# Optimization experiments

Hardware: AMD Instinct MI355X
Metric: run time of the kernel (lower is better)

Reference implementation:

```python
import jax, jax.numpy as jnp
import numpy as np

B, S, E = 1, 2048, 2048
HQ, HKV = 32, 8
D = E // HQ            # 64 head dim
REP = HQ // HKV        # 4 q-heads per kv-head
NEG = -1e9


def _rope(t, fr, fi):
    # t: [B,S,H,D]; fr/fi: [S,D//2] real/imag of unit complex freqs
    tr = t.reshape(*t.shape[:-1], D // 2, 2)
    t0, t1 = tr[..., 0], tr[..., 1]
    fr = fr[None, :, None, :]
    fi = fi[None, :, None, :]
    out = jnp.stack([t0 * fr - t1 * fi, t0 * fi + t1 * fr], axis=-1)
    return out.reshape(t.shape)


def setup_inputs() -> dict:
    key = jax.random.key(0)
    kx, kq, kk, kv, ko = jax.random.split(key, 5)
    x = jax.random.normal(kx, (B, S, E), dtype=jnp.float32)
    # standard RoPE frequencies: theta = 10000^{-2i/D}
    inv_freq = 1.0 / (10000.0 ** (np.arange(0, D, 2, dtype=np.float32) / D))
    ang = np.arange(S, dtype=np.float32)[:, None] * inv_freq[None, :]  # [S, D//2]
    freqs_cis = jnp.asarray(np.stack([np.cos(ang), np.sin(ang)], axis=-1))  # [S,D//2,2]
    # causal additive mask [S,S]
    mask = jnp.where(np.tril(np.ones((S, S), dtype=bool)), 0.0, NEG).astype(jnp.float32)
    s = 1.0 / np.sqrt(E)
    Wq = jax.random.normal(kq, (E, HQ * D), dtype=jnp.float32) * s
    Wk = jax.random.normal(kk, (E, HKV * D), dtype=jnp.float32) * s
    Wv = jax.random.normal(kv, (E, HKV * D), dtype=jnp.float32) * s
    Wo = jax.random.normal(ko, (HQ * D, E), dtype=jnp.float32) * s
    return {"x": x, "freqs_cis": freqs_cis, "mask": mask,
            "Wq": Wq, "Wk": Wk, "Wv": Wv, "Wo": Wo}


def reference(x, freqs_cis, mask, Wq, Wk, Wv, Wo):
    b, s, _ = x.shape
    xq = (x @ Wq).reshape(b, s, HQ, D)
    xk = (x @ Wk).reshape(b, s, HKV, D)
    xv = (x @ Wv).reshape(b, s, HKV, D)
    fr, fi = freqs_cis[..., 0], freqs_cis[..., 1]
    xq = _rope(xq, fr, fi)
    xk = _rope(xk, fr, fi)
    # explicit GQA kv-head repeat (matches torch repeat+view)
    xk = jnp.repeat(xk, REP, axis=2)  # [b,s,HQ,D]
    xv = jnp.repeat(xv, REP, axis=2)
    q = xq.transpose(0, 2, 1, 3)  # [b,h,s,d]
    k = xk.transpose(0, 2, 1, 3)
    v = xv.transpose(0, 2, 1, 3)
    scores = jnp.einsum('bhqd,bhkd->bhqk', q, k) / jnp.sqrt(jnp.float32(D))
    scores = scores + mask[None, None]
    probs = jax.nn.softmax(scores, axis=-1)
    attn = jnp.einsum('bhqk,bhkd->bhqd', probs, v)
    attn = attn.transpose(0, 2, 1, 3).reshape(b, s, HQ * D)
    return attn @ Wo
```

## Files before the change

kernel.cpp:

```cpp
#include <hip/hip_runtime.h>
#include <stdint.h>

#define SEQ   2048
#define EDIM  2048
#define NHQ   32
#define NHKV  8
#define HDIM  64
#define NQKV  3072

#define LOG2E 1.4426950408889634f

typedef __bf16 bf16x8 __attribute__((ext_vector_type(8)));
typedef float  f32x4  __attribute__((ext_vector_type(4)));

typedef __attribute__((address_space(1))) void gvoid;
typedef __attribute__((address_space(3))) void lvoid;

__device__ __forceinline__ unsigned short f2bf(float f) {
  unsigned int u = __builtin_bit_cast(unsigned int, f);
  u += 0x7FFFu + ((u >> 16) & 1u);
  return (unsigned short)(u >> 16);
}

__device__ __forceinline__ unsigned int pk2bf(float lo, float hi) {
  return (unsigned)f2bf(lo) | ((unsigned)f2bf(hi) << 16);
}

__device__ __forceinline__ float fexp2(float x) {
#if __has_builtin(__builtin_amdgcn_exp2f)
  return __builtin_amdgcn_exp2f(x);
#else
  return exp2f(x);
#endif
}

__device__ __forceinline__ bf16x8 ld_g16(const unsigned short* p) {
  uint4 u = *reinterpret_cast<const uint4*>(p);
  return __builtin_bit_cast(bf16x8, u);
}

__device__ __forceinline__ void stage16(const void* g, void* l) {
  __builtin_amdgcn_global_load_lds((gvoid*)g, (lvoid*)l, 16, 0, 0);
}

__global__ __launch_bounds__(256) void conv_x_kernel(
    const float* __restrict__ x, unsigned short* __restrict__ xb) {
  int i = (blockIdx.x * 256 + threadIdx.x) * 8;
  float4 a = *reinterpret_cast<const float4*>(x + i);
  float4 b = *reinterpret_cast<const float4*>(x + i + 4);
  uint4 o;
  o.x = pk2bf(a.x, a.y);
  o.y = pk2bf(a.z, a.w);
  o.z = pk2bf(b.x, b.y);
  o.w = pk2bf(b.z, b.w);
  *reinterpret_cast<uint4*>(xb + i) = o;
}

__global__ __launch_bounds__(256) void tr_qkv_kernel(
    const float* __restrict__ Wq, const float* __restrict__ Wk,
    const float* __restrict__ Wv, unsigned short* __restrict__ Bt) {
  __shared__ float tile[32][33];
  const int tx = threadIdx.x, ty = threadIdx.y;
  const int kb = blockIdx.x * 32, nb = blockIdx.y * 32;
#pragma unroll
  for (int i = 0; i < 4; ++i) {
    int k = kb + ty + i * 8;
    int n = nb + tx;
    float v;
    if (n < 2048)      v = Wq[k * 2048 + n];
    else if (n < 2560) v = Wk[k * 512 + (n - 2048)];
    else               v = Wv[k * 512 + (n - 2560)];
    tile[ty + i * 8][tx] = v;
  }
  __syncthreads();
#pragma unroll
  for (int i = 0; i < 4; ++i) {
    int n = nb + ty + i * 8;
    int k = kb + tx;
    Bt[n * 2048 + k] = f2bf(tile[tx][ty + i * 8]);
  }
}

__global__ __launch_bounds__(256) void tr_wo_kernel(
    const float* __restrict__ Wo, unsigned short* __restrict__ Bt) {
  __shared__ float tile[32][33];
  const int tx = threadIdx.x, ty = threadIdx.y;
  const int kb = blockIdx.x * 32, nb = blockIdx.y * 32;
#pragma unroll
  for (int i = 0; i < 4; ++i)
    tile[ty + i * 8][tx] = Wo[(kb + ty + i * 8) * 2048 + nb + tx];
  __syncthreads();
#pragma unroll
  for (int i = 0; i < 4; ++i)
    Bt[(nb + ty + i * 8) * 2048 + kb + tx] = f2bf(tile[tx][ty + i * 8]);
}

template <int MODE>
__global__ __launch_bounds__(256) void gemm_kernel(
    const unsigned short* __restrict__ A, const unsigned short* __restrict__ Bt,
    const float* __restrict__ freqs, unsigned short* __restrict__ Qb,
    unsigned short* __restrict__ Kb, unsigned short* __restrict__ VT,
    float* __restrict__ Cout, int N_, int K) {
  __shared__ alignas(16) unsigned short As[2][128 * 32];
  __shared__ alignas(16) unsigned short Bs[2][128 * 32];
  const int t = threadIdx.x;
  const int w = t >> 6, l = t & 63;
  const int q = l >> 4, r16 = l & 15;
  const int wr = w >> 1, wc = w & 1;
  const int brow = blockIdx.x * 128, bcol = blockIdx.y * 128;
  const unsigned short* Arow = A + (size_t)brow * K;
  const unsigned short* Brow = Bt + (size_t)bcol * K;
  const int sg0 = t, sg1 = 256 + t;
  f32x4 acc[4][4] = {};

  {
    stage16(Arow + (sg0 >> 2) * K + (sg0 & 3) * 8, (char*)As[0] + sg0 * 16);
    stage16(Brow + (sg0 >> 2) * K + (sg0 & 3) * 8, (char*)Bs[0] + sg0 * 16);
    stage16(Arow + (sg1 >> 2) * K + (sg1 & 3) * 8, (char*)As[0] + sg1 * 16);
    stage16(Brow + (sg1 >> 2) * K + (sg1 & 3) * 8, (char*)Bs[0] + sg1 * 16);
  }
  __syncthreads();

  for (int kt = 0; kt < K; kt += 32) {
    const int cur = (kt >> 5) & 1;
    if (kt + 32 < K) {
      const int nkt = kt + 32;
      stage16(Arow + (sg0 >> 2) * K + nkt + (sg0 & 3) * 8,
              (char*)As[cur ^ 1] + sg0 * 16);
      stage16(Brow + (sg0 >> 2) * K + nkt + (sg0 & 3) * 8,
              (char*)Bs[cur ^ 1] + sg0 * 16);
      stage16(Arow + (sg1 >> 2) * K + nkt + (sg1 & 3) * 8,
              (char*)As[cur ^ 1] + sg1 * 16);
      stage16(Brow + (sg1 >> 2) * K + nkt + (sg1 & 3) * 8,
              (char*)Bs[cur ^ 1] + sg1 * 16);
    }
    bf16x8 af[4], bfr[4];
#pragma unroll
    for (int mf = 0; mf < 4; ++mf)
      af[mf] = *(const bf16x8*)(As[cur] + (wr * 64 + mf * 16 + r16) * 32 + q * 8);
#pragma unroll
    for (int nf = 0; nf < 4; ++nf)
      bfr[nf] = *(const bf16x8*)(Bs[cur] + (wc * 64 + nf * 16 + r16) * 32 + q * 8);
#pragma unroll
    for (int mf = 0; mf < 4; ++mf)
#pragma unroll
      for (int nf = 0; nf < 4; ++nf)
        acc[mf][nf] = __builtin_amdgcn_mfma_f32_16x16x32_bf16(
            af[mf], bfr[nf], acc[mf][nf], 0, 0, 0);
    __syncthreads();
  }

#pragma unroll
  for (int mf = 0; mf < 4; ++mf) {
#pragma unroll
    for (int nf = 0; nf < 4; ++nf) {
      int j = bcol + wc * 64 + nf * 16 + r16;
#pragma unroll
      for (int reg = 0; reg < 4; ++reg) {
        float v = acc[mf][nf][reg];
        int srow = brow + wr * 64 + mf * 16 + q * 4 + reg;
        if (MODE == 1) {
          Cout[(size_t)srow * N_ + j] = v;
        } else {
          float pv = __shfl_xor(v, 1);
          int d = j & 63;
          if (j < 2048) {
            float2 f = *reinterpret_cast<const float2*>(
                freqs + ((size_t)srow * 32 + (d >> 1)) * 2);
            float ov = (d & 1) ? (pv * f.y + v * f.x) : (v * f.x - pv * f.y);
            Qb[(size_t)(j >> 6) * (SEQ * HDIM) + srow * HDIM + d] =
                f2bf(ov * (0.125f * LOG2E));
          } else if (j < 2560) {
            float2 f = *reinterpret_cast<const float2*>(
                freqs + ((size_t)srow * 32 + (d >> 1)) * 2);
            float ov = (d & 1) ? (pv * f.y + v * f.x) : (v * f.x - pv * f.y);
            Kb[(size_t)((j - 2048) >> 6) * (SEQ * HDIM) + srow * HDIM + d] =
                f2bf(ov);
          } else {
            VT[(size_t)((j - 2560) >> 6) * (HDIM * SEQ) + d * SEQ + srow] =
                f2bf(v);
          }
        }
      }
    }
  }
}

__global__ __launch_bounds__(64, 3) void flash_kernel(
    const unsigned short* __restrict__ Qb, const unsigned short* __restrict__ Kb,
    const unsigned short* __restrict__ VT, unsigned short* __restrict__ attnb) {
  const int bi = blockIdx.x;
  const int h = bi & 31, hk = h >> 2;
  const int qc = 63 - (bi >> 5);
  const int l = threadIdx.x & 63;
  const int hi = l >> 4, r16 = l & 15;
  const int qrow0 = qc * 32;
  const unsigned short* Qh = Qb + (size_t)h * (SEQ * HDIM);
  const unsigned short* Kh = Kb + (size_t)hk * (SEQ * HDIM);
  const unsigned short* Vh = VT + (size_t)hk * (HDIM * SEQ);

  bf16x8 qf[2][2];
#pragma unroll
  for (int mf = 0; mf < 2; ++mf)
#pragma unroll
    for (int ks = 0; ks < 2; ++ks)
      qf[mf][ks] = ld_g16(Qh + (qrow0 + mf * 16 + r16) * HDIM + ks * 32 + hi * 8);

  f32x4 o[2][4] = {};
  float mrow[2] = {-1e9f, -1e9f};
  float lrow[2] = {0.f, 0.f};

  const int nkv = (qc >> 2) + 1;
  for (int kv = 0; kv < nkv; ++kv) {
    const int kvbase = kv * 128;
    f32x4 s[2][8] = {};
#pragma unroll
    for (int nf = 0; nf < 8; ++nf) {
      const unsigned short* kp =
          Kh + (size_t)(kvbase + nf * 16 + r16) * HDIM + hi * 8;
      bf16x8 a0 = ld_g16(kp);
      bf16x8 a1 = ld_g16(kp + 32);
      s[0][nf] = __builtin_amdgcn_mfma_f32_16x16x32_bf16(a0, qf[0][0], s[0][nf], 0, 0, 0);
      s[1][nf] = __builtin_amdgcn_mfma_f32_16x16x32_bf16(a0, qf[1][0], s[1][nf], 0, 0, 0);
      s[0][nf] = __builtin_amdgcn_mfma_f32_16x16x32_bf16(a1, qf[0][1], s[0][nf], 0, 0, 0);
      s[1][nf] = __builtin_amdgcn_mfma_f32_16x16x32_bf16(a1, qf[1][1], s[1][nf], 0, 0, 0);
    }
    if (kv == nkv - 1) {
#pragma unroll
      for (int mf = 0; mf < 2; ++mf) {
        int qr = qrow0 + mf * 16 + r16;
#pragma unroll
        for (int nf = 0; nf < 8; ++nf) {
          int kc = kvbase + nf * 16 + hi * 4;
#pragma unroll
          for (int r = 0; r < 4; ++r)
            if (kc + r > qr) s[mf][nf][r] = -1e9f;
        }
      }
    }
    float mx[2];
#pragma unroll
    for (int mf = 0; mf < 2; ++mf) {
      f32x4 m4 = s[mf][0];
#pragma unroll
      for (int nf = 1; nf < 8; ++nf) {
        m4[0] = fmaxf(m4[0], s[mf][nf][0]); m4[1] = fmaxf(m4[1], s[mf][nf][1]);
        m4[2] = fmaxf(m4[2], s[mf][nf][2]); m4[3] = fmaxf(m4[3], s[mf][nf][3]);
      }
      float v = fmaxf(fmaxf(m4[0], m4[1]), fmaxf(m4[2], m4[3]));
      v = fmaxf(v, __shfl_xor(v, 16));
      v = fmaxf(v, __shfl_xor(v, 32));
      mx[mf] = v;
    }
    if (!__all(fmaxf(mx[0] - mrow[0], mx[1] - mrow[1]) <= 8.0f)) {
#pragma unroll
      for (int mf = 0; mf < 2; ++mf) {
        float mn = fmaxf(mrow[mf], mx[mf]);
        float al = fexp2(mrow[mf] - mn);
        mrow[mf] = mn;
        lrow[mf] *= al;
#pragma unroll
        for (int r = 0; r < 4; ++r) {
          float alr = __shfl(al, hi * 4 + r);
#pragma unroll
          for (int nd = 0; nd < 4; ++nd) o[mf][nd][r] *= alr;
        }
      }
    }
#pragma unroll
    for (int mf = 0; mf < 2; ++mf) {
      f32x4 a4 = {0.f, 0.f, 0.f, 0.f};
#pragma unroll
      for (int nf = 0; nf < 8; ++nf) {
#pragma unroll
        for (int r = 0; r < 4; ++r) {
          float p = fexp2(s[mf][nf][r] - mrow[mf]);
          s[mf][nf][r] = p;
          a4[r] += p;
        }
      }
      float rs = (a4[0] + a4[1]) + (a4[2] + a4[3]);
      rs += __shfl_xor(rs, 16);
      rs += __shfl_xor(rs, 32);
      lrow[mf] += rs;
    }
#pragma unroll
    for (int kt = 0; kt < 8; ++kt) {
      bf16x8 pa[2];
#pragma unroll
      for (int mf = 0; mf < 2; ++mf) {
        bf16x8 p = {};
        p[0] = (__bf16)s[mf][kt][0];
        p[1] = (__bf16)s[mf][kt][1];
        p[2] = (__bf16)s[mf][kt][2];
        p[3] = (__bf16)s[mf][kt][3];
        pa[mf] = p;
      }
#pragma unroll
      for (int nd = 0; nd < 4; ++nd) {
        uint2 v2 = *reinterpret_cast<const uint2*>(
            Vh + (size_t)(nd * 16 + r16) * SEQ + kvbase + kt * 16 + hi * 4);
        uint4 u; u.x = v2.x; u.y = v2.y; u.z = 0u; u.w = 0u;
        bf16x8 vb = __builtin_bit_cast(bf16x8, u);
        o[0][nd] = __builtin_amdgcn_mfma_f32_16x16x32_bf16(pa[0], vb, o[0][nd], 0, 0, 0);
        o[1][nd] = __builtin_amdgcn_mfma_f32_16x16x32_bf16(pa[1], vb, o[1][nd], 0, 0, 0);
      }
    }
  }
#pragma unroll
  for (int mf = 0; mf < 2; ++mf) {
    float linv = 1.0f / lrow[mf];
#pragma unroll
    for (int r = 0; r < 4; ++r) {
      float lr = __shfl(linv, hi * 4 + r);
      int srow = qrow0 + mf * 16 + hi * 4 + r;
#pragma unroll
      for (int nd = 0; nd < 4; ++nd) {
        int d = nd * 16 + r16;
        attnb[(size_t)srow * 2048 + h * 64 + d] = f2bf(o[mf][nd][r] * lr);
      }
    }
  }
}

extern "C" void kernel_launch(void* const* d_in, const int* in_sizes, int n_in,
                              void* d_out, int out_size, void* d_ws,
                              size_t ws_size, hipStream_t stream) {
  const float* x     = (const float*)d_in[0];
  const float* freqs = (const float*)d_in[1];
  const float* Wq = (const float*)d_in[3];
  const float* Wk = (const float*)d_in[4];
  const float* Wv = (const float*)d_in[5];
  const float* Wo = (const float*)d_in[6];
  float* out = (float*)d_out;
  char* ws = (char*)d_ws;
  const size_t MB = 1024 * 1024;
  unsigned short* xb    = (unsigned short*)(ws);
  unsigned short* WqkvT = (unsigned short*)(ws + 8 * MB);
  unsigned short* WoT   = (unsigned short*)(ws + 20 * MB);
  unsigned short* Qbuf  = (unsigned short*)(ws + 28 * MB);
  unsigned short* Kbuf  = (unsigned short*)(ws + 36 * MB);
  unsigned short* Vt    = (unsigned short*)(ws + 38 * MB);
  unsigned short* attnb = (unsigned short*)(ws + 40 * MB);

  conv_x_kernel<<<dim3(2048), dim3(256), 0, stream>>>(x, xb);
  tr_qkv_kernel<<<dim3(64, 96), dim3(32, 8), 0, stream>>>(Wq, Wk, Wv, WqkvT);
  tr_wo_kernel<<<dim3(64, 64), dim3(32, 8), 0, stream>>>(Wo, WoT);
  gemm_kernel<0><<<dim3(16, 24), dim3(256), 0, stream>>>(
      xb, WqkvT, freqs, Qbuf, Kbuf, Vt, (float*)nullptr, NQKV, 2048);
  flash_kernel<<<dim3(2048), dim3(64), 0, stream>>>(Qbuf, Kbuf, Vt, attnb);
  gemm_kernel<1><<<dim3(16, 16), dim3(256), 0, stream>>>(
      attnb, WoT, (const float*)nullptr, (unsigned short*)nullptr,
      (unsigned short*)nullptr, (unsigned short*)nullptr, out, 2048, 2048);
}
```

Baseline: 357.2 us.

## Retile GEMMs to 128x64 with K=64 steps, XOR-swizzled LDS, XCD block remap

The projection GEMMs now use 128x64 output tiles with a 64-deep K step instead of 128x128 with a 32-deep step. The LDS layout gets an XOR swizzle to avoid bank conflicts. A 1D grid is remapped so consecutive tiles land on the same XCD, which should improve L2 reuse. Smaller N tiles double the block count (768/512), which fills the 256 CUs better, at the cost of less register reuse per block.

```diff
diff --git a/kernel.cpp b/kernel.cpp
--- a/kernel.cpp
+++ b/kernel.cpp
@@ -100,61 +100,73 @@
     const unsigned short* __restrict__ A, const unsigned short* __restrict__ Bt,
     const float* __restrict__ freqs, unsigned short* __restrict__ Qb,
     unsigned short* __restrict__ Kb, unsigned short* __restrict__ VT,
-    float* __restrict__ Cout, int N_, int K) {
-  __shared__ alignas(16) unsigned short As[2][128 * 32];
-  __shared__ alignas(16) unsigned short Bs[2][128 * 32];
+    float* __restrict__ Cout, int N_, int K, int nwg) {
+  __shared__ alignas(16) unsigned short As[2][128 * 64];
+  __shared__ alignas(16) unsigned short Bs[2][64 * 64];
   const int t = threadIdx.x;
   const int w = t >> 6, l = t & 63;
   const int q = l >> 4, r16 = l & 15;
   const int wr = w >> 1, wc = w & 1;
-  const int brow = blockIdx.x * 128, bcol = blockIdx.y * 128;
+  const int cpx = nwg >> 3;
+  const int id = (blockIdx.x & 7) * cpx + (blockIdx.x >> 3);
+  const int brow = (id & 15) * 128;
+  const int bcol = (id >> 4) * 64;
   const unsigned short* Arow = A + (size_t)brow * K;
   const unsigned short* Brow = Bt + (size_t)bcol * K;
-  const int sg0 = t, sg1 = 256 + t;
-  f32x4 acc[4][4] = {};
-
-  {
-    stage16(Arow + (sg0 >> 2) * K + (sg0 & 3) * 8, (char*)As[0] + sg0 * 16);
-    stage16(Brow + (sg0 >> 2) * K + (sg0 & 3) * 8, (char*)Bs[0] + sg0 * 16);
-    stage16(Arow + (sg1 >> 2) * K + (sg1 & 3) * 8, (char*)As[0] + sg1 * 16);
-    stage16(Brow + (sg1 >> 2) * K + (sg1 & 3) * 8, (char*)Bs[0] + sg1 * 16);
-  }
+  f32x4 acc[4][2] = {};
+
+#define STAGE_TILE(buf, ktb)                                                  \
+  {                                                                           \
+    _Pragma("unroll") for (int it = 0; it < 4; ++it) {                        \
+      int sg = it * 256 + t;                                                  \
+      int row = sg >> 3, ks = sg & 7;                                         \
+      stage16(Arow + (size_t)row * K + (ktb) + ((ks ^ (row & 7)) << 3),       \
+              (char*)As[buf] + sg * 16);                                      \
+    }                                                                         \
+    _Pragma("unroll") for (int it = 0; it < 2; ++it) {                        \
+      int sg = it * 256 + t;                                                  \
+      int row = sg >> 3, ks = sg & 7;                                         \
+      stage16(Brow + (size_t)row * K + (ktb) + ((ks ^ (row & 7)) << 3),       \
+              (char*)Bs[buf] + sg * 16);                                      \
+    }                                                                         \
+  }
+
+  STAGE_TILE(0, 0)
   __syncthreads();
 
-  for (int kt = 0; kt < K; kt += 32) {
-    const int cur = (kt >> 5) & 1;
-    if (kt + 32 < K) {
-      const int nkt = kt + 32;
-      stage16(Arow + (sg0 >> 2) * K + nkt + (sg0 & 3) * 8,
-              (char*)As[cur ^ 1] + sg0 * 16);
-      stage16(Brow + (sg0 >> 2) * K + nkt + (sg0 & 3) * 8,
-              (char*)Bs[cur ^ 1] + sg0 * 16);
-      stage16(Arow + (sg1 >> 2) * K + nkt + (sg1 & 3) * 8,
-              (char*)As[cur ^ 1] + sg1 * 16);
-      stage16(Brow + (sg1 >> 2) * K + nkt + (sg1 & 3) * 8,
-              (char*)Bs[cur ^ 1] + sg1 * 16);
-    }
-    bf16x8 af[4], bfr[4];
-#pragma unroll
-    for (int mf = 0; mf < 4; ++mf)
-      af[mf] = *(const bf16x8*)(As[cur] + (wr * 64 + mf * 16 + r16) * 32 + q * 8);
-#pragma unroll
-    for (int nf = 0; nf < 4; ++nf)
-      bfr[nf] = *(const bf16x8*)(Bs[cur] + (wc * 64 + nf * 16 + r16) * 32 + q * 8);
-#pragma unroll
-    for (int mf = 0; mf < 4; ++mf)
-#pragma unroll
-      for (int nf = 0; nf < 4; ++nf)
-        acc[mf][nf] = __builtin_amdgcn_mfma_f32_16x16x32_bf16(
-            af[mf], bfr[nf], acc[mf][nf], 0, 0, 0);
+  for (int kt = 0; kt < K; kt += 64) {
+    const int cur = (kt >> 6) & 1;
+    if (kt + 64 < K) STAGE_TILE(cur ^ 1, kt + 64)
+#pragma unroll
+    for (int kk = 0; kk < 2; ++kk) {
+      bf16x8 af[4], bfr[2];
+#pragma unroll
+      for (int mf = 0; mf < 4; ++mf) {
+        int arow = wr * 64 + mf * 16 + r16;
+        int slot = ((kk << 2) + q) ^ (arow & 7);
+        af[mf] = *(const bf16x8*)(As[cur] + arow * 64 + slot * 8);
+      }
+#pragma unroll
+      for (int nf = 0; nf < 2; ++nf) {
+        int brw = wc * 32 + nf * 16 + r16;
+        int slot = ((kk << 2) + q) ^ (brw & 7);
+        bfr[nf] = *(const bf16x8*)(Bs[cur] + brw * 64 + slot * 8);
+      }
+#pragma unroll
+      for (int mf = 0; mf < 4; ++mf)
+#pragma unroll
+        for (int nf = 0; nf < 2; ++nf)
+          acc[mf][nf] = __builtin_amdgcn_mfma_f32_16x16x32_bf16(
+              af[mf], bfr[nf], acc[mf][nf], 0, 0, 0);
+    }
     __syncthreads();
   }
 
 #pragma unroll
   for (int mf = 0; mf < 4; ++mf) {
 #pragma unroll
-    for (int nf = 0; nf < 4; ++nf) {
-      int j = bcol + wc * 64 + nf * 16 + r16;
+    for (int nf = 0; nf < 2; ++nf) {
+      int j = bcol + wc * 32 + nf * 16 + r16;
 #pragma unroll
       for (int reg = 0; reg < 4; ++reg) {
         float v = acc[mf][nf][reg];
@@ -184,6 +196,7 @@
       }
     }
   }
+#undef STAGE_TILE
 }
 
 __global__ __launch_bounds__(64, 3) void flash_kernel(
@@ -346,10 +359,10 @@
   conv_x_kernel<<<dim3(2048), dim3(256), 0, stream>>>(x, xb);
   tr_qkv_kernel<<<dim3(64, 96), dim3(32, 8), 0, stream>>>(Wq, Wk, Wv, WqkvT);
   tr_wo_kernel<<<dim3(64, 64), dim3(32, 8), 0, stream>>>(Wo, WoT);
-  gemm_kernel<0><<<dim3(16, 24), dim3(256), 0, stream>>>(
-      xb, WqkvT, freqs, Qbuf, Kbuf, Vt, (float*)nullptr, NQKV, 2048);
+  gemm_kernel<0><<<dim3(768), dim3(256), 0, stream>>>(
+      xb, WqkvT, freqs, Qbuf, Kbuf, Vt, (float*)nullptr, NQKV, 2048, 768);
   flash_kernel<<<dim3(2048), dim3(64), 0, stream>>>(Qbuf, Kbuf, Vt, attnb);
-  gemm_kernel<1><<<dim3(16, 16), dim3(256), 0, stream>>>(
+  gemm_kernel<1><<<dim3(512), dim3(256), 0, stream>>>(
       attnb, WoT, (const float*)nullptr, (unsigned short*)nullptr,
-      (unsigned short*)nullptr, (unsigned short*)nullptr, out, 2048, 2048);
-}
+      (unsigned short*)nullptr, (unsigned short*)nullptr, out, 2048, 2048, 512);
+}
```

Measured after the change: 325.8 us. -8.8%, faster.
